# Kernel optimization log

Measured on AMD Instinct MI355X. Metric: run time of the kernel, lower is better.

## Reference

```python
import jax, jax.numpy as jnp
import numpy as np

EPS = 1e-6
BETA = 0.5
B, T, N = 128, 30, 10000   # batch, BP iterations, n error bits
M, K = 5000, 10            # checks, observables
CHK_W, OBS_W = 6, 50       # row weights of chkmat / obsmat


def _make_supports():
    """Deterministic sparse supports (CSR-style flattened col indices + row ids)."""
    rng = np.random.default_rng(0)
    chk_rows = np.argpartition(rng.random((M, N)), CHK_W, axis=1)[:, :CHK_W]
    obs_rows = np.argpartition(rng.random((K, N)), OBS_W, axis=1)[:, :OBS_W]
    chk_idx = chk_rows.reshape(-1).astype(np.int32)
    chk_seg = np.repeat(np.arange(M, dtype=np.int32), CHK_W)
    obs_idx = obs_rows.reshape(-1).astype(np.int32)
    obs_seg = np.repeat(np.arange(K, dtype=np.int32), OBS_W)
    return chk_idx, chk_seg, obs_idx, obs_seg


def setup_inputs() -> dict:
    key = jax.random.key(0)
    k1, k2, k3 = jax.random.split(key, 3)
    all_llrs = jax.random.normal(k1, (B, T, N), dtype=jnp.float32) * 2.0
    syndromes = jax.random.randint(k2, (B, M), 0, 2, dtype=jnp.int32)
    observables = jax.random.randint(k3, (B, K), 0, 2, dtype=jnp.int32)
    chk_idx, chk_seg, obs_idx, obs_seg = _make_supports()
    return {
        "all_llrs": all_llrs,
        "syndromes": syndromes,
        "observables": observables,
        "chk_idx": jnp.asarray(chk_idx),
        "chk_seg": jnp.asarray(chk_seg),
        "obs_idx": jnp.asarray(obs_idx),
        "obs_seg": jnp.asarray(obs_seg),
    }


def _pred_llr(t, idx, seg, num_seg):
    # t: (B,T,N) tanh(llr/2); gather support cols -> (B,T,E)
    g = t[:, :, idx]
    # segmented product over support entries (tanh rule), segments on axis 0
    p = jax.ops.segment_prod(jnp.moveaxis(g, 2, 0), seg, num_segments=num_seg)  # (S,B,T)
    p = jnp.clip(jnp.moveaxis(p, 0, 2), -1.0 + EPS, 1.0 - EPS)  # (B,T,S)
    return 2.0 * jnp.arctanh(p)


def _bce_with_logits(z, y):
    # stable BCEWithLogits: max(z,0) - z*y + log(1+exp(-|z|)) == logaddexp(0,z) - z*y
    return jnp.logaddexp(0.0, z) - z * y


def reference(all_llrs, syndromes, observables, chk_idx, chk_seg, obs_idx, obs_seg):
    t = jnp.tanh(all_llrs * 0.5)                                   # (B,T,N)
    syn_llr = _pred_llr(t, chk_idx, chk_seg, syndromes.shape[1])    # (B,T,M)
    obs_llr = _pred_llr(t, obs_idx, obs_seg, observables.shape[1])  # (B,T,K)
    y_syn = syndromes.astype(jnp.float32)[:, None, :]
    y_obs = observables.astype(jnp.float32)[:, None, :]
    loss1 = _bce_with_logits(-syn_llr, y_syn).sum(axis=2)           # (B,T)
    loss2 = _bce_with_logits(-obs_llr, y_obs).sum(axis=2)           # (B,T)
    loss = BETA * loss1 + (1.0 - BETA) * loss2
    return loss.mean()
```

## Files before the change

### kernel.cpp

```cpp
#include <hip/hip_runtime.h>

typedef float floatx2 __attribute__((ext_vector_type(2)));

#define B_  128
#define T_  30
#define N_  10000
#define M_  5000
#define K_  10
#define OBS_W_ 50
#define EPS_ 1e-6f
#define LOG2F_ 0.69314718056f
#define BT_  3840
#define CHUNK_ 100
#define NCHK_ (M_/CHUNK_)
#define NB_ 10

__device__ __forceinline__ float tanh_half(float x) {
    float r = __builtin_amdgcn_rcpf(__expf(x) + 1.f);
    return __builtin_fmaf(-2.f, r, 1.f);
}

__global__ __launch_bounds__(256) void tanh_transpose_fp8(
    const float*   __restrict__ llrs,
    unsigned char* __restrict__ tt)
{
    __shared__ float tile[64][65];
    const int bt0 = blockIdx.x * 64;
    const int n0  = blockIdx.y * 64;
    const int tid = threadIdx.x;

    #pragma unroll
    for (int i = 0; i < 4; ++i) {
        int lin = i * 256 + tid;
        int r   = lin >> 4;
        int c4  = (lin & 15) * 4;
        if (n0 + c4 < N_) {
            float4 v = *(const float4*)(llrs + (size_t)(bt0 + r) * N_ + n0 + c4);
            tile[r][c4 + 0] = tanh_half(v.x);
            tile[r][c4 + 1] = tanh_half(v.y);
            tile[r][c4 + 2] = tanh_half(v.z);
            tile[r][c4 + 3] = tanh_half(v.w);
        }
    }
    __syncthreads();

    const int q  = tid & 15;
    const int cg = tid >> 4;
    #pragma unroll
    for (int i = 0; i < 4; ++i) {
        int col = cg + 16 * i;
        if (n0 + col < N_) {
            float v0 = tile[4 * q + 0][col];
            float v1 = tile[4 * q + 1][col];
            float v2 = tile[4 * q + 2][col];
            float v3 = tile[4 * q + 3][col];
            int pk = __builtin_amdgcn_cvt_pk_fp8_f32(v0, v1, 0, false);
            pk     = __builtin_amdgcn_cvt_pk_fp8_f32(v2, v3, pk, true);
            *(int*)(tt + (size_t)(n0 + col) * BT_ + bt0 + 4 * q) = pk;
        }
    }
}

__device__ __forceinline__ void cvt4(unsigned int qv, float* a) {
    floatx2 lo = __builtin_amdgcn_cvt_pk_f32_fp8((int)qv, false);
    floatx2 hi = __builtin_amdgcn_cvt_pk_f32_fp8((int)qv, true);
    a[0] = lo.x; a[1] = lo.y; a[2] = hi.x; a[3] = hi.y;
}

__global__ __launch_bounds__(256) void gather_loss_fp8(
    const unsigned char* __restrict__ tt,
    const int*           __restrict__ syndromes,
    const int*           __restrict__ observables,
    const int*           __restrict__ chk_idx,
    const int*           __restrict__ obs_idx,
    float*               __restrict__ out)
{
    __shared__ int   sidx[CHUNK_ * 6];
    __shared__ int   ssyn[NB_][CHUNK_];
    __shared__ float red[4];

    const int tid  = threadIdx.x;
    const int lane = tid & 63;
    const int wave = tid >> 6;
    const int r0   = blockIdx.x * 256 + lane * 4;
    const int bA   = r0 / 30;
    const int bB   = (r0 + 3) / 30;
    const int split= (bA + 1) * 30 - r0;
    const int b_lo = (blockIdx.x * 256) / 30;
    const unsigned char* col0 = tt + r0;
    const int y = blockIdx.y;
    float acc = 0.f;

    if (y < NCHK_) {
        const int m0 = y * CHUNK_;
        for (int i = tid; i < CHUNK_ * 6; i += 256)
            sidx[i] = chk_idx[m0 * 6 + i];
        for (int i = tid; i < NB_ * CHUNK_; i += 256) {
            int bi = i / CHUNK_, j = i - bi * CHUNK_;
            int b  = b_lo + bi; if (b > B_ - 1) b = B_ - 1;
            ((int*)ssyn)[i] = syndromes[(size_t)b * M_ + m0 + j];
        }
        __syncthreads();
        const int iA = bA - b_lo, iB = bB - b_lo;

        #pragma unroll 2
        for (int s = wave * 25; s < wave * 25 + 25; ++s) {
            int i0 = sidx[s * 6 + 0], i1 = sidx[s * 6 + 1], i2 = sidx[s * 6 + 2];
            int i3 = sidx[s * 6 + 3], i4 = sidx[s * 6 + 4], i5 = sidx[s * 6 + 5];
            unsigned int q0 = *(const unsigned int*)(col0 + (size_t)i0 * BT_);
            unsigned int q1 = *(const unsigned int*)(col0 + (size_t)i1 * BT_);
            unsigned int q2 = *(const unsigned int*)(col0 + (size_t)i2 * BT_);
            unsigned int q3 = *(const unsigned int*)(col0 + (size_t)i3 * BT_);
            unsigned int q4 = *(const unsigned int*)(col0 + (size_t)i4 * BT_);
            unsigned int q5 = *(const unsigned int*)(col0 + (size_t)i5 * BT_);
            float a[4], b4[4], p[4];
            cvt4(q0, p);  cvt4(q1, a);  cvt4(q2, b4);
            #pragma unroll
            for (int j = 0; j < 4; ++j) p[j] *= a[j] * b4[j];
            cvt4(q3, a);  cvt4(q4, b4);
            #pragma unroll
            for (int j = 0; j < 4; ++j) p[j] *= a[j] * b4[j];
            cvt4(q5, a);
            float sgA = ssyn[iA][s] ? -1.f : 1.f;
            float sgB = ssyn[iB][s] ? -1.f : 1.f;
            #pragma unroll
            for (int j = 0; j < 4; ++j) {
                float sg = (j >= split) ? sgB : sgA;
                float sp = sg * p[j] * a[j];
                sp = fminf(fmaxf(sp, -1.f + EPS_), 1.f - EPS_);
                acc += LOG2F_ - __logf(1.f + sp);
            }
        }
    } else {
        for (int k = wave; k < K_; k += 4) {
            const int* oi = obs_idx + k * OBS_W_;
            float p[4] = {1.f, 1.f, 1.f, 1.f};
            #pragma unroll 5
            for (int j2 = 0; j2 < OBS_W_; ++j2) {
                unsigned int qq = *(const unsigned int*)(col0 + (size_t)oi[j2] * BT_);
                float a[4];
                cvt4(qq, a);
                p[0] *= a[0]; p[1] *= a[1]; p[2] *= a[2]; p[3] *= a[3];
            }
            float sgA = observables[(size_t)bA * K_ + k] ? -1.f : 1.f;
            float sgB = observables[(size_t)bB * K_ + k] ? -1.f : 1.f;
            #pragma unroll
            for (int j = 0; j < 4; ++j) {
                float sg = (j >= split) ? sgB : sgA;
                float sp = sg * p[j];
                sp = fminf(fmaxf(sp, -1.f + EPS_), 1.f - EPS_);
                acc += LOG2F_ - __logf(1.f + sp);
            }
        }
    }

    #pragma unroll
    for (int off = 32; off > 0; off >>= 1)
        acc += __shfl_down(acc, off, 64);
    if (lane == 0) red[wave] = acc;
    __syncthreads();
    if (tid == 0) {
        float s = red[0] + red[1] + red[2] + red[3];
        atomicAdd(out, s * (0.5f / (float)BT_));
    }
}

extern "C" void kernel_launch(void* const* d_in, const int* in_sizes, int n_in,
                              void* d_out, int out_size, void* d_ws, size_t ws_size,
                              hipStream_t stream) {
    const float* all_llrs    = (const float*)d_in[0];
    const int*   syndromes   = (const int*)d_in[1];
    const int*   observables = (const int*)d_in[2];
    const int*   chk_idx     = (const int*)d_in[3];
    const int*   obs_idx     = (const int*)d_in[5];
    float*         out = (float*)d_out;
    unsigned char* tt  = (unsigned char*)d_ws;

    hipMemsetAsync(out, 0, sizeof(float) * out_size, stream);

    dim3 g1(BT_ / 64, (N_ + 63) / 64);
    tanh_transpose_fp8<<<g1, 256, 0, stream>>>(all_llrs, tt);

    dim3 g2(BT_ / 256, NCHK_ + 1);
    gather_loss_fp8<<<g2, 256, 0, stream>>>(
        tt, syndromes, observables, chk_idx, obs_idx, out);
}
```

Before: 275.6 us.

## Pack fp8 before LDS and widen transpose tile to 256 rows

The tanh/transpose kernel now converts to fp8 in registers before the LDS stage, keeping packed 4-row words in shared memory instead of floats. Each block covers 256 bt rows, so every output column write becomes a 16-byte store instead of a 4-byte one. The aim is to cut LDS traffic and make the global stores to the transposed fp8 buffer wider and fewer. The trade-off is a quarter as many blocks and more registers per thread for the 4x4 staging.

```diff
diff --git a/kernel.cpp b/kernel.cpp
--- a/kernel.cpp
+++ b/kernel.cpp
@@ -24,39 +24,48 @@
     const float*   __restrict__ llrs,
     unsigned char* __restrict__ tt)
 {
-    __shared__ float tile[64][65];
-    const int bt0 = blockIdx.x * 64;
+    __shared__ unsigned int lds[64][65];
+    const int bt0 = blockIdx.x * 256;
     const int n0  = blockIdx.y * 64;
     const int tid = threadIdx.x;
+    const int c4  = tid & 15;
+    const int r4b = tid >> 4;
 
     #pragma unroll
-    for (int i = 0; i < 4; ++i) {
-        int lin = i * 256 + tid;
-        int r   = lin >> 4;
-        int c4  = (lin & 15) * 4;
-        if (n0 + c4 < N_) {
-            float4 v = *(const float4*)(llrs + (size_t)(bt0 + r) * N_ + n0 + c4);
-            tile[r][c4 + 0] = tanh_half(v.x);
-            tile[r][c4 + 1] = tanh_half(v.y);
-            tile[r][c4 + 2] = tanh_half(v.z);
-            tile[r][c4 + 3] = tanh_half(v.w);
+    for (int it = 0; it < 4; ++it) {
+        const int r4 = r4b + 16 * it;
+        if (n0 + 4 * c4 < N_) {
+            float t[4][4];
+            #pragma unroll
+            for (int j = 0; j < 4; ++j) {
+                float4 v = *(const float4*)(llrs +
+                            (size_t)(bt0 + 4 * r4 + j) * N_ + n0 + 4 * c4);
+                t[j][0] = tanh_half(v.x);
+                t[j][1] = tanh_half(v.y);
+                t[j][2] = tanh_half(v.z);
+                t[j][3] = tanh_half(v.w);
+            }
+            #pragma unroll
+            for (int k = 0; k < 4; ++k) {
+                int pk = __builtin_amdgcn_cvt_pk_fp8_f32(t[0][k], t[1][k], 0, false);
+                pk     = __builtin_amdgcn_cvt_pk_fp8_f32(t[2][k], t[3][k], pk, true);
+                lds[r4][4 * c4 + k] = (unsigned int)pk;
+            }
         }
     }
     __syncthreads();
 
-    const int q  = tid & 15;
-    const int cg = tid >> 4;
+    const int w = tid & 15;
     #pragma unroll
-    for (int i = 0; i < 4; ++i) {
-        int col = cg + 16 * i;
+    for (int it = 0; it < 4; ++it) {
+        const int col = (tid >> 4) + 16 * it;
         if (n0 + col < N_) {
-            float v0 = tile[4 * q + 0][col];
-            float v1 = tile[4 * q + 1][col];
-            float v2 = tile[4 * q + 2][col];
-            float v3 = tile[4 * q + 3][col];
-            int pk = __builtin_amdgcn_cvt_pk_fp8_f32(v0, v1, 0, false);
-            pk     = __builtin_amdgcn_cvt_pk_fp8_f32(v2, v3, pk, true);
-            *(int*)(tt + (size_t)(n0 + col) * BT_ + bt0 + 4 * q) = pk;
+            uint4 d;
+            d.x = lds[4 * w + 0][col];
+            d.y = lds[4 * w + 1][col];
+            d.z = lds[4 * w + 2][col];
+            d.w = lds[4 * w + 3][col];
+            *(uint4*)(tt + (size_t)(n0 + col) * BT_ + bt0 + 16 * w) = d;
         }
     }
 }
@@ -178,7 +187,7 @@
 
     hipMemsetAsync(out, 0, sizeof(float) * out_size, stream);
 
-    dim3 g1(BT_ / 64, (N_ + 63) / 64);
+    dim3 g1(BT_ / 256, (N_ + 63) / 64);
     tanh_transpose_fp8<<<g1, 256, 0, stream>>>(all_llrs, tt);
 
     dim3 g2(BT_ / 256, NCHK_ + 1);
```

After: 268.6 us. -2.5%, faster.
